# Performance work log

Hardware: AMD Instinct MI355X
Metric: run time of the kernel (lower is better)

Reference implementation:

```python
import jax, jax.numpy as jnp
import numpy as np

DELTA = 1e-6  # small constant used throughout the original repo


def _theta(memory, keys):
    # batchwise cosine similarity: memory [b,m,w], keys [b,r,w] -> [b,r,m]
    a = memory / (jnp.linalg.norm(memory, axis=2, keepdims=True) + DELTA)
    b = keys / (jnp.linalg.norm(keys, axis=2, keepdims=True) + DELTA)
    return jnp.einsum('bmw,brw->brm', a, b)


def _content_weightings(memory, keys, strengths):
    d = _theta(memory, keys)                       # [b,r,m]
    s = jax.nn.softplus(strengths)[..., None]      # [b,r,1]
    return jax.nn.softmax(d * s, axis=2)


def _allocate(usage):
    # usage [b,m]
    u = DELTA + (1.0 - DELTA) * usage
    phi = jnp.argsort(u, axis=1)                          # ascending, like topk(largest=False)
    sorted_u = jnp.take_along_axis(u, phi, axis=1)
    sorted_alloc = (1.0 - sorted_u) * jnp.cumprod(sorted_u, axis=1)  # fake_cumprod == inclusive cumprod
    alloc = jnp.take_along_axis(sorted_alloc, phi, axis=1)           # faithful to .gather(1, phi) in source
    return alloc[:, None, :]                              # [b,1,m]


def _dnc_step(xi, W, bW, memory, link_matrix, precedence, read_weights, write_weights, usage_vector):
    b, m, w = memory.shape
    r = read_weights.shape[1]
    iface = xi @ W + bW                                   # [b, r*w + 3*w + 5*r + 3]
    i0 = r * w
    read_keys = iface[:, :i0].reshape(b, r, w)
    read_strengths = 1.0 + jax.nn.relu(iface[:, i0:i0 + r])              # [b,r]
    write_key = iface[:, i0 + r:i0 + r + w].reshape(b, 1, w)
    write_strength = (1.0 + jax.nn.relu(iface[:, i0 + r + w]))[:, None]  # [b,1]
    erase_vector = jax.nn.sigmoid(iface[:, i0 + r + w + 1:i0 + r + 2 * w + 1]).reshape(b, 1, w)
    write_vector = iface[:, i0 + r + 2 * w + 1:i0 + r + 3 * w + 1].reshape(b, 1, w)
    free_gates = jax.nn.sigmoid(iface[:, i0 + r + 3 * w + 1:i0 + 2 * r + 3 * w + 1])  # [b,r]
    allocation_gate = jax.nn.sigmoid(iface[:, i0 + 2 * r + 3 * w + 1])[:, None]       # [b,1]
    write_gate = jax.nn.sigmoid(iface[:, i0 + 2 * r + 3 * w + 2])[:, None]            # [b,1]
    # NOTE: source slices read_modes starting at the write_gate index (faithful) and softmaxes over dim 1
    read_modes = jax.nn.softmax(iface[:, i0 + 2 * r + 3 * w + 2:i0 + 5 * r + 3 * w + 2].reshape(b, r, 3), axis=1)

    # ---- write path ----
    usage = usage_vector + (1.0 - usage_vector) * (1.0 - jnp.prod(1.0 - write_weights, axis=1))
    psi = jnp.prod(1.0 - free_gates[:, :, None] * read_weights, axis=1)  # [b,m]
    usage = usage * psi

    write_content_w = _content_weightings(memory, write_key, write_strength)  # [b,1,m]
    alloc = _allocate(usage)                                                  # [b,1,m]
    ag = allocation_gate[:, :, None]
    wg = write_gate[:, :, None]
    new_write_w = wg * (ag * alloc + (1.0 - ag) * write_content_w)            # [b,1,m]

    weighted_resets = new_write_w[:, :, :, None] * erase_vector[:, :, None, :]  # [b,1,m,w]
    reset_gate = jnp.prod(1.0 - weighted_resets, axis=1)                        # [b,m,w]
    new_memory = memory * reset_gate + jnp.einsum('bkm,bkw->bmw', new_write_w, write_vector)

    prec4 = precedence[:, :, None, :]            # [b,1,1,m]
    ww_i = new_write_w[:, :, :, None]            # [b,1,m,1]
    ww_j = new_write_w[:, :, None, :]            # [b,1,1,m]
    new_link = (1.0 - ww_i - ww_j) * link_matrix + ww_i * prec4
    new_link = new_link * (1.0 - jnp.eye(m, dtype=memory.dtype))[None, None]

    new_prec = (1.0 - jnp.sum(new_write_w, axis=2, keepdims=True)) * precedence + new_write_w

    # ---- read path ----
    content_w = _content_weightings(new_memory, read_keys, read_strengths)  # [b,r,m]
    forward_w = jnp.einsum('bkmn,brn->brkm', new_link, read_weights)        # [b,r,1,m]
    backward_w = jnp.einsum('brm,bkmn->brkn', read_weights, new_link)       # [b,r,1,m]
    content_mode = read_modes[:, :, 2:3] * content_w
    backward_mode = jnp.sum(read_modes[:, :, 0:1, None] * backward_w, axis=2)
    forward_mode = jnp.sum(read_modes[:, :, 1:2, None] * forward_w, axis=2)
    new_read_w = backward_mode + content_mode + forward_mode                # [b,r,m]

    read_vectors = jnp.einsum('brm,bmw->brw', new_read_w, new_memory)       # [b,r,w]
    return read_vectors


def setup_inputs() -> dict:
    key = jax.random.key(0)
    ks = jax.random.split(key, 3)
    b, m, w, r, d = 64, 1024, 64, 4, 512
    iface_size = r * w + 3 * w + 5 * r + 3  # 471
    return {
        'xi': jax.random.normal(ks[0], (b, d), dtype=jnp.float32),
        'W': jax.random.normal(ks[1], (d, iface_size), dtype=jnp.float32) * 0.05,
        'bW': jnp.zeros((iface_size,), dtype=jnp.float32),
        'memory': jnp.zeros((b, m, w), dtype=jnp.float32),
        'link_matrix': jnp.zeros((b, 1, m, m), dtype=jnp.float32),
        'precedence': jnp.zeros((b, 1, m), dtype=jnp.float32),
        'read_weights': jnp.zeros((b, r, m), dtype=jnp.float32),
        'write_weights': jnp.zeros((b, 1, m), dtype=jnp.float32),
        'usage_vector': jnp.zeros((b, m), dtype=jnp.float32),
    }


def reference(xi, W, bW, memory, link_matrix, precedence, read_weights, write_weights, usage_vector):
    return _dnc_step(xi, W, bW, memory, link_matrix, precedence, read_weights, write_weights, usage_vector)
```

## Files before the change

kernel.cpp:

```cpp
#include <hip/hip_runtime.h>

#define DELTA 1e-6f

#define NB 64
#define NM 1024
#define NW 64
#define NR 4
#define ND 512
#define NIF 471

typedef unsigned long long ull;

__device__ __forceinline__ float sigmoidf_(float x){ return 1.0f/(1.0f+expf(-x)); }
__device__ __forceinline__ float softplusf_(float x){ return fmaxf(x,0.0f) + log1pf(expf(-fabsf(x))); }

__device__ __forceinline__ float waveSum(float v){
  #pragma unroll
  for(int o=32;o>0;o>>=1) v += __shfl_down(v,o,64);
  return v;
}
__device__ __forceinline__ float waveMax(float v){
  #pragma unroll
  for(int o=32;o>0;o>>=1) v = fmaxf(v, __shfl_down(v,o,64));
  return v;
}
__device__ __forceinline__ ull shflxor64(ull k, int m){
  unsigned lo = (unsigned)(k & 0xffffffffu), hi = (unsigned)(k>>32);
  lo = (unsigned)__shfl_xor((int)lo, m, 64);
  hi = (unsigned)__shfl_xor((int)hi, m, 64);
  return ((ull)hi<<32)|lo;
}

__global__ __launch_bounds__(256) void k_zero(float4* __restrict__ p, int n4){
  int i = blockIdx.x*256 + threadIdx.x;
  if (i < n4) p[i] = make_float4(0.f,0.f,0.f,0.f);
}

__global__ __launch_bounds__(256) void k_iface(const float* __restrict__ xi,
                                               const float* __restrict__ Wm,
                                               const float* __restrict__ bW,
                                               float* __restrict__ iface){
  int b = blockIdx.x, half = blockIdx.y;
  __shared__ float xs[ND];
  for(int k=threadIdx.x;k<ND;k+=256) xs[k]=xi[b*ND+k];
  __syncthreads();
  int c = half*236 + threadIdx.x;
  int cend = half ? NIF : 236;
  if (c < cend){
    float acc = bW[c];
    #pragma unroll 4
    for(int k=0;k<ND;k++) acc = fmaf(xs[k], Wm[k*NIF+c], acc);
    iface[b*NIF+c]=acc;
  }
}

__global__ __launch_bounds__(256) void k_wcos(
    const float* __restrict__ iface, const float* __restrict__ mem,
    const float* __restrict__ rw_old, const float* __restrict__ ww_old,
    const float* __restrict__ uv,
    float* __restrict__ uu, float* __restrict__ wcd, float* __restrict__ wcn){
  int b = blockIdx.y;
  int j = blockIdx.x*256 + threadIdx.x;
  __shared__ float wkey[NW];
  const float* ifb = iface + b*NIF;
  if (threadIdx.x < NW) wkey[threadIdx.x] = ifb[260+threadIdx.x];
  __syncthreads();
  float fg0=sigmoidf_(ifb[453]), fg1=sigmoidf_(ifb[454]);
  float fg2=sigmoidf_(ifb[455]), fg3=sigmoidf_(ifb[456]);
  float u0  = uv[b*NM+j];
  float wwo = ww_old[b*NM+j];
  float usage = u0 + (1.0f-u0)*wwo;
  float psi = (1.0f - fg0*rw_old[(b*NR+0)*NM+j])
            * (1.0f - fg1*rw_old[(b*NR+1)*NM+j])
            * (1.0f - fg2*rw_old[(b*NR+2)*NM+j])
            * (1.0f - fg3*rw_old[(b*NR+3)*NM+j]);
  usage *= psi;
  uu[b*NM+j] = DELTA + (1.0f-DELTA)*usage;
  float dot=0.0f, nrm=0.0f;
  const float4* mrow4 = (const float4*)(mem + ((size_t)b*NM + j)*NW);
  #pragma unroll 4
  for(int k=0;k<16;k++){
    float4 mv = mrow4[k];
    const float* wk = wkey + k*4;
    dot = fmaf(mv.x,wk[0],dot); dot = fmaf(mv.y,wk[1],dot);
    dot = fmaf(mv.z,wk[2],dot); dot = fmaf(mv.w,wk[3],dot);
    nrm = fmaf(mv.x,mv.x,nrm); nrm = fmaf(mv.y,mv.y,nrm);
    nrm = fmaf(mv.z,mv.z,nrm); nrm = fmaf(mv.w,mv.w,nrm);
  }
  wcd[b*NM+j]=dot; wcn[b*NM+j]=nrm;
}

__global__ __launch_bounds__(1024) void k_write2(
    const float* __restrict__ iface, const float* __restrict__ uu,
    const float* __restrict__ wcd, const float* __restrict__ wcn,
    float* __restrict__ wwp){
  int b = blockIdx.x; int tid = threadIdx.x;
  int lane = tid & 63, wv = tid >> 6;
  __shared__ float wkey[NW];
  __shared__ ull skA[NM];
  __shared__ ull skB[NM];
  __shared__ float fb2[NM];
  __shared__ float red[17];
  __shared__ float s_wp[16], s_wp2[16];
  const float* ifb = iface + b*NIF;
  if (tid < NW) wkey[tid] = ifb[260+tid];
  __syncthreads();
  float sw = softplusf_(1.0f + fmaxf(ifb[324],0.0f));
  float ag = sigmoidf_(ifb[457]);
  float wg = sigmoidf_(ifb[458]);
  float kn=0.0f;
  for(int k=0;k<NW;k++){ float t=wkey[k]; kn += t*t; }
  kn = sqrtf(kn);
  float logit = sw * wcd[b*NM+tid] / ((sqrtf(wcn[b*NM+tid])+DELTA)*(kn+DELTA));
  float m1 = waveMax(logit); if(lane==0) red[wv]=m1; __syncthreads();
  if(tid==0){ float mm=red[0]; for(int i=1;i<16;i++) mm=fmaxf(mm,red[i]); red[16]=mm; } __syncthreads();
  float e = expf(logit - red[16]);
  float s1 = waveSum(e); if(lane==0) red[wv]=s1; __syncthreads();
  if(tid==0){ float ss=0; for(int i=0;i<16;i++) ss+=red[i]; red[16]=ss; } __syncthreads();
  float wcw = e/red[16];
  float u = uu[b*NM+tid];
  ull k = ((ull)__float_as_uint(u) << 32) | (unsigned)tid;
  bool useA = true;
  for (int k2=2; k2<=NM; k2<<=1){
    for (int jj=k2>>1; jj>0; jj>>=1){
      ull p;
      if (jj >= 64){
        ull* buf = useA ? skA : skB;
        buf[tid] = k;
        __syncthreads();
        p = buf[tid^jj];
        useA = !useA;
      } else {
        p = shflxor64(k, jj);
      }
      bool lower = (tid & jj) == 0;
      bool asc   = (tid & k2) == 0;
      bool takeMin = (lower == asc);
      k = takeMin ? (k<p ? k : p) : (k>p ? k : p);
    }
  }
  float su = __uint_as_float((unsigned)(k>>32));
  int phi  = (int)(k & 0xffffffffu);
  float sc = su;
  #pragma unroll
  for (int off=1; off<64; off<<=1){
    float t = __shfl_up(sc, off, 64);
    if (lane >= off) sc *= t;
  }
  if (lane==63) s_wp[wv] = sc;
  __syncthreads();
  if (tid==0){
    float p=1.0f;
    for (int w=0;w<16;w++){ float t=s_wp[w]; s_wp2[w]=p; p*=t; }
  }
  __syncthreads();
  float P = sc * s_wp2[wv];
  float salloc = (1.0f - su)*P;
  fb2[phi] = salloc;
  __syncthreads();
  float alloc = fb2[tid];
  wwp[b*NM+tid] = wg*(ag*alloc + (1.0f-ag)*wcw);
}

__global__ __launch_bounds__(256) void k_link8(
    const float* __restrict__ link, const float* __restrict__ rw,
    const float* __restrict__ wwp,
    float4* __restrict__ RFp, float* __restrict__ C2p, float* __restrict__ C3p,
    float* __restrict__ ldiag){
  int cx = blockIdx.x, ry = blockIdx.y, b = blockIdx.z;
  int tid = threadIdx.x, lane = tid&63, wv = tid>>6;
  __shared__ float4 s_L4[32*64];
  __shared__ float4 s_gcol4[256];
  __shared__ float  s_mwc[256];
  __shared__ float4 s_grow4[32];
  __shared__ float  s_wwr[32];
  __shared__ float4 s_rfp4[128];
  const float* Lb = link + ((size_t)b<<20);
  int colbase = cx*256, rowbase = ry*256;
  {
    float g0 = rw[(b*NR+0)*NM + colbase + tid];
    float g1 = rw[(b*NR+1)*NM + colbase + tid];
    float g2 = rw[(b*NR+2)*NM + colbase + tid];
    float g3 = rw[(b*NR+3)*NM + colbase + tid];
    s_gcol4[tid] = make_float4(g0,g1,g2,g3);
    s_mwc[tid] = 1.0f - wwp[b*NM + colbase + tid];
  }
  float c2a[NR][4], c3a[NR][4];
  #pragma unroll
  for(int r=0;r<NR;r++){
    #pragma unroll
    for(int e=0;e<4;e++){ c2a[r][e]=0.0f; c3a[r][e]=0.0f; }
  }
  for (int ch=0; ch<8; ++ch){
    int rb = rowbase + ch*32;
    if (tid < 128) ((float*)s_grow4)[tid] = rw[(b*NR+(tid&3))*NM + rb + (tid>>2)];
    if (tid < 32)  s_wwr[tid] = wwp[b*NM + rb + tid];
    #pragma unroll
    for (int jq=0;jq<8;jq++){
      int rl = wv + 4*jq;
      float4 lv = *(const float4*)(Lb + (size_t)(rb+rl)*NM + colbase + lane*4);
      s_L4[rl*64 + (lane ^ ((rl>>1)&7))] = lv;
    }
    __syncthreads();
    if (cx == ry && tid < 32){
      int coff = ch*32 + tid;
      float4 v = s_L4[tid*64 + ((coff>>2) ^ ((tid>>1)&7))];
      float d = (coff&1) ? ((coff&2)? v.w : v.y) : ((coff&2)? v.z : v.x);
      ldiag[b*NM + rb + tid] = d;
    }
    {
      int i5 = lane & 15, cg = lane >> 4;
      int rl0 = 2*i5;
      int sz = i5 & 7;
      float wwj0 = s_wwr[rl0], wwj1 = s_wwr[rl0+1];
      float rf0[4] = {0,0,0,0}, rf1[4] = {0,0,0,0};
      #pragma unroll
      for (int q=0;q<4;q++){
        int cq = wv*16 + cg*4 + q;
        float4 mw  = ((const float4*)s_mwc)[cq];
        float4 lv0 = s_L4[rl0*64 + (cq ^ sz)];
        float4 lv1 = s_L4[(rl0+1)*64 + (cq ^ sz)];
        float le0[4]={lv0.x,lv0.y,lv0.z,lv0.w};
        float le1[4]={lv1.x,lv1.y,lv1.z,lv1.w};
        float mv[4]={mw.x,mw.y,mw.z,mw.w};
        #pragma unroll
        for (int e=0;e<4;e++){
          float4 gv = s_gcol4[cq*4+e];
          float lt0 = le0[e]*(mv[e]-wwj0);
          float lt1 = le1[e]*(mv[e]-wwj1);
          rf0[0]=fmaf(lt0,gv.x,rf0[0]); rf0[1]=fmaf(lt0,gv.y,rf0[1]);
          rf0[2]=fmaf(lt0,gv.z,rf0[2]); rf0[3]=fmaf(lt0,gv.w,rf0[3]);
          rf1[0]=fmaf(lt1,gv.x,rf1[0]); rf1[1]=fmaf(lt1,gv.y,rf1[1]);
          rf1[2]=fmaf(lt1,gv.z,rf1[2]); rf1[3]=fmaf(lt1,gv.w,rf1[3]);
        }
      }
      #pragma unroll
      for (int r=0;r<NR;r++){
        rf0[r] += __shfl_xor(rf0[r], 16, 64);
        rf0[r] += __shfl_xor(rf0[r], 32, 64);
        rf1[r] += __shfl_xor(rf1[r], 16, 64);
        rf1[r] += __shfl_xor(rf1[r], 32, 64);
      }
      if (cg == 0){
        s_rfp4[wv*32 + rl0]     = make_float4(rf0[0],rf0[1],rf0[2],rf0[3]);
        s_rfp4[wv*32 + rl0 + 1] = make_float4(rf1[0],rf1[1],rf1[2],rf1[3]);
      }
    }
    #pragma unroll 2
    for (int ri=0; ri<8; ri++){
      int row = wv*8 + ri;
      float4 lv = s_L4[row*64 + (lane ^ ((row>>1)&7))];
      float4 gg = s_grow4[row];
      float wwr = s_wwr[row];
      float le[4] = {lv.x,lv.y,lv.z,lv.w};
      float ggv[4] = {gg.x,gg.y,gg.z,gg.w};
      float ggw[4];
      #pragma unroll
      for (int r=0;r<NR;r++) ggw[r] = ggv[r]*wwr;
      #pragma unroll
      for (int e=0;e<4;e++){
        #pragma unroll
        for (int r=0;r<NR;r++){
          c2a[r][e] = fmaf(le[e], ggv[r], c2a[r][e]);
          c3a[r][e] = fmaf(le[e], ggw[r], c3a[r][e]);
        }
      }
    }
    __syncthreads();
    if (tid < 128){
      int row = tid>>2, r = tid&3;
      float s = ((const float*)&s_rfp4[0*32+row])[r] + ((const float*)&s_rfp4[1*32+row])[r]
              + ((const float*)&s_rfp4[2*32+row])[r] + ((const float*)&s_rfp4[3*32+row])[r];
      ((float*)RFp)[((size_t)cx<<18) + (b*NM + rb + row)*4 + r] = s;
    }
    __syncthreads();
  }
  float4* s_comb = s_L4;
  #pragma unroll
  for (int r=0;r<NR;r++){
    s_comb[tid*8 + r]     = make_float4(c2a[r][0],c2a[r][1],c2a[r][2],c2a[r][3]);
    s_comb[tid*8 + 4 + r] = make_float4(c3a[r][0],c3a[r][1],c3a[r][2],c3a[r][3]);
  }
  __syncthreads();
  for (int t=tid; t<512; t+=256){
    int lc = t>>3, q = t&7;
    float4 a = s_comb[(0*64+lc)*8+q];
    float4 bb= s_comb[(1*64+lc)*8+q];
    float4 c = s_comb[(2*64+lc)*8+q];
    float4 d = s_comb[(3*64+lc)*8+q];
    float4 s = make_float4(a.x+bb.x+c.x+d.x, a.y+bb.y+c.y+d.y, a.z+bb.z+c.z+d.z, a.w+bb.w+c.w+d.w);
    float* dst = (q<4) ? &C2p[((size_t)ry<<18) + (b*NR+q)*NM + colbase + lc*4]
                       : &C3p[((size_t)ry<<18) + (b*NR+(q-4))*NM + colbase + lc*4];
    *(float4*)dst = s;
  }
}

__global__ __launch_bounds__(256) void k_rdots(
    const float* __restrict__ iface, const float* __restrict__ mem,
    const float* __restrict__ wwp, float* __restrict__ dots){
  int b = blockIdx.y;
  int j = blockIdx.x*256 + threadIdx.x;
  __shared__ float keys[NR][NW];
  __shared__ float er[NW], wvec[NW];
  const float* ifb = iface + b*NIF;
  { int r=threadIdx.x>>6, kk=threadIdx.x&63; keys[r][kk] = ifb[r*NW+kk]; }
  if (threadIdx.x < 64) er[threadIdx.x] = sigmoidf_(ifb[325+threadIdx.x]);
  else if (threadIdx.x < 128) wvec[threadIdx.x-64] = ifb[389+threadIdx.x-64];
  __syncthreads();
  float wwj = wwp[b*NM+j];
  const float* mrow = mem + ((size_t)b*NM+j)*NW;
  float dt[NR]={0,0,0,0}; float nrm=0.0f;
  for(int k=0;k<NW;k++){
    float nmv = fmaf(mrow[k], (1.0f - wwj*er[k]), wwj*wvec[k]);
    nrm = fmaf(nmv,nmv,nrm);
    #pragma unroll
    for(int r=0;r<NR;r++) dt[r] = fmaf(nmv, keys[r][k], dt[r]);
  }
  #pragma unroll
  for(int r=0;r<NR;r++) dots[(b*5+r)*NM + j] = dt[r];
  dots[(b*5+4)*NM + j] = nrm;
}

__global__ __launch_bounds__(1024) void k_rmid(
    const float* __restrict__ iface, const float* __restrict__ prec,
    const float* __restrict__ rw_old, const float* __restrict__ wwp,
    const float* __restrict__ dots, const float* __restrict__ ldiag,
    const float4* __restrict__ RFp4, const float* __restrict__ C2p, const float* __restrict__ C3p,
    float* __restrict__ nrwg){
  int b = blockIdx.x; int tid = threadIdx.x; int lane=tid&63, wv=tid>>6;
  __shared__ float s_pk[16][8];
  __shared__ float scal[16];
  __shared__ float smax[NR], ssum[NR];
  __shared__ float rm[NR][3];
  const float* ifb = iface + b*NIF;
  if (tid == 0){
    for(int mo=0;mo<3;mo++){
      float x0=ifb[458+0*3+mo], x1=ifb[458+1*3+mo], x2=ifb[458+2*3+mo], x3=ifb[458+3*3+mo];
      float mx = fmaxf(fmaxf(x0,x1),fmaxf(x2,x3));
      float e0=expf(x0-mx),e1=expf(x1-mx),e2=expf(x2-mx),e3=expf(x3-mx);
      float s=e0+e1+e2+e3;
      rm[0][mo]=e0/s; rm[1][mo]=e1/s; rm[2][mo]=e2/s; rm[3][mo]=e3/s;
    }
  }
  if (tid >= 320 && tid < 324){
    int r = tid-320;
    float knv=0;
    for(int k=0;k<NW;k++){ float t=ifb[r*NW+k]; knv += t*t; }
    scal[8+r]  = sqrtf(knv);
    scal[12+r] = softplusf_(1.0f + fmaxf(ifb[256+r],0.0f));
  }
  __syncthreads();
  int j = tid;
  float pj  = prec[b*NM+j];
  float wwj = wwp[b*NM+j];
  float rwv[NR];
  #pragma unroll
  for(int r=0;r<NR;r++) rwv[r]=rw_old[(b*NR+r)*NM+j];
  {
    float v8[8];
    #pragma unroll
    for(int r=0;r<NR;r++){ v8[r] = pj*rwv[r]; v8[4+r] = wwj*rwv[r]; }
    #pragma unroll
    for(int q=0;q<8;q++){
      float s = waveSum(v8[q]);
      if(lane==0) s_pk[wv][q]=s;
    }
    __syncthreads();
    if (tid < 8){
      float ss=0;
      for(int w=0;w<16;w++) ss += s_pk[w][tid];
      scal[tid]=ss;
    }
    __syncthreads();
  }
  float dt[NR];
  #pragma unroll
  for(int r=0;r<NR;r++) dt[r] = dots[(b*5+r)*NM + j];
  float nrm = dots[(b*5+4)*NM + j];
  float inv = 1.0f/(sqrtf(nrm)+DELTA);
  float logit[NR], ce[NR], cw[NR];
  #pragma unroll
  for(int r=0;r<NR;r++) logit[r] = scal[12+r]*dt[r]*inv/(scal[8+r]+DELTA);
  #pragma unroll
  for(int r=0;r<NR;r++){
    float m1 = waveMax(logit[r]);
    if(lane==0) s_pk[wv][r]=m1;
  }
  __syncthreads();
  if (tid < NR){
    float mm=s_pk[0][tid];
    for(int w=1;w<16;w++) mm=fmaxf(mm,s_pk[w][tid]);
    smax[tid]=mm;
  }
  __syncthreads();
  #pragma unroll
  for(int r=0;r<NR;r++){
    ce[r] = expf(logit[r]-smax[r]);
    float s1 = waveSum(ce[r]);
    if(lane==0) s_pk[wv][r]=s1;
  }
  __syncthreads();
  if (tid < NR){
    float ss=0;
    for(int w=0;w<16;w++) ss += s_pk[w][tid];
    ssum[tid]=ss;
  }
  __syncthreads();
  #pragma unroll
  for(int r=0;r<NR;r++) cw[r] = ce[r]/ssum[r];
  float Ljj = ldiag[b*NM+j];
  float4 Fa = RFp4[(0<<16) + b*NM + j];
  float4 Fb = RFp4[(1<<16) + b*NM + j];
  float4 Fc = RFp4[(2<<16) + b*NM + j];
  float4 Fd = RFp4[(3<<16) + b*NM + j];
  float Fr[4] = {Fa.x+Fb.x+Fc.x+Fd.x, Fa.y+Fb.y+Fc.y+Fd.y,
                 Fa.z+Fb.z+Fc.z+Fd.z, Fa.w+Fb.w+Fc.w+Fd.w};
  #pragma unroll
  for(int r=0;r<NR;r++){
    int idx = (b*NR+r)*NM + j;
    float cc2 = C2p[idx] + C2p[262144+idx] + C2p[524288+idx] + C2p[786432+idx];
    float cc3 = C3p[idx] + C3p[262144+idx] + C3p[524288+idx] + C3p[786432+idx];
    float F   = Fr[r];
    float grj = rwv[r];
    float fwd = F - Ljj*grj*(1.0f-2.0f*wwj) + wwj*(scal[r] - pj*grj);
    float bwd = (cc2 - cc3) - Ljj*grj*(1.0f-wwj) - wwj*(cc2 - Ljj*grj) + pj*(scal[4+r] - wwj*grj);
    nrwg[(b*NR+r)*NM+j] = rm[r][0]*bwd + rm[r][1]*fwd + rm[r][2]*cw[r];
  }
}

__global__ __launch_bounds__(256) void k_readb(
    const float* __restrict__ iface, const float* __restrict__ mem,
    const float* __restrict__ wwp, const float* __restrict__ nrwg,
    float* __restrict__ out){
  int jt = blockIdx.x, b = blockIdx.y;
  int tid = threadIdx.x, lane = tid&63, wv = tid>>6;
  __shared__ float s_nrw[NR][256];
  __shared__ float s_ww[256];
  __shared__ float s_er[NW], s_wv[NW];
  __shared__ float s_acc[4][NR][NW];
  const float* ifb = iface + b*NIF;
  int j0 = jt*256;
  #pragma unroll
  for(int r=0;r<NR;r++) s_nrw[r][tid] = nrwg[(b*NR+r)*NM + j0+tid];
  s_ww[tid] = wwp[b*NM + j0+tid];
  if (tid < 64) s_er[tid] = sigmoidf_(ifb[325+tid]);
  else if (tid < 128) s_wv[tid-64] = ifb[389+tid-64];
  __syncthreads();
  int w = lane;
  float erw = s_er[w], wvw = s_wv[w];
  float acc[NR]={0,0,0,0};
  for(int jj=0;jj<64;jj++){
    int jl = wv*64+jj;
    float wwr = s_ww[jl];
    float nmv = fmaf(mem[((size_t)b*NM + j0+jl)*NW + w], (1.0f - wwr*erw), wwr*wvw);
    #pragma unroll
    for(int r=0;r<NR;r++) acc[r] = fmaf(s_nrw[r][jl], nmv, acc[r]);
  }
  #pragma unroll
  for(int r=0;r<NR;r++) s_acc[wv][r][w] = acc[r];
  __syncthreads();
  {
    int r = tid>>6, k = tid&63;
    float s = s_acc[0][r][k]+s_acc[1][r][k]+s_acc[2][r][k]+s_acc[3][r][k];
    atomicAdd(&out[b*NR*NW + r*NW + k], s);
  }
}

extern "C" void kernel_launch(void* const* d_in, const int* in_sizes, int n_in,
                              void* d_out, int out_size, void* d_ws, size_t ws_size,
                              hipStream_t stream) {
  (void)in_sizes; (void)n_in; (void)out_size; (void)ws_size;
  const float* xi   = (const float*)d_in[0];
  const float* Wm   = (const float*)d_in[1];
  const float* bW   = (const float*)d_in[2];
  const float* mem  = (const float*)d_in[3];
  const float* link = (const float*)d_in[4];
  const float* prec = (const float*)d_in[5];
  const float* rw   = (const float*)d_in[6];
  const float* wwo  = (const float*)d_in[7];
  const float* uv   = (const float*)d_in[8];
  float* out = (float*)d_out;
  float* ws  = (float*)d_ws;
  float* iface = ws;
  float* wwp   = ws + 30208;
  float* uu    = ws + 95744;
  float* wcd   = ws + 161280;
  float* wcn   = ws + 226816;
  float* dots  = ws + 292352;
  float* ldiag = ws + 620032;
  float* nrwg  = ws + 685568;
  float* RFp   = ws + 947712;
  float* C2p   = ws + 1996288;
  float* C3p   = ws + 3044864;
  k_zero <<<16, 256, 0, stream>>>((float4*)out, 4096);
  k_iface<<<dim3(NB,2), 256, 0, stream>>>(xi, Wm, bW, iface);
  k_wcos <<<dim3(4,NB), 256, 0, stream>>>(iface, mem, rw, wwo, uv, uu, wcd, wcn);
  k_write2<<<NB, 1024, 0, stream>>>(iface, uu, wcd, wcn, wwp);
  k_link8<<<dim3(4,4,NB), 256, 0, stream>>>(link, rw, wwp, (float4*)RFp, C2p, C3p, ldiag);
  k_rdots<<<dim3(4,NB), 256, 0, stream>>>(iface, mem, wwp, dots);
  k_rmid <<<NB, 1024, 0, stream>>>(iface, prec, rw, wwp, dots, ldiag, (const float4*)RFp, C2p, C3p, nrwg);
  k_readb<<<dim3(4,NB), 256, 0, stream>>>(iface, mem, wwp, nrwg, out);
}
```

Before: 158.6 us.

## Fuse read-dot and output-zero kernels into link kernel with smaller row chunks

Merges the k_rdots and k_zero launches into the link kernel by adding an extra grid slice (blockIdx.y==4) that computes memory-key dot products and zeroes the output. The link tile loop now processes 16-row chunks instead of 32, preloads all row gates and write weights once, and halves shared-memory use for the link tile. This removes two launches, lets the dot-product blocks overlap with link work, and raises occupancy, at the cost of more loop iterations and barriers per block.

```diff
diff --git a/kernel.cpp b/kernel.cpp
--- a/kernel.cpp
+++ b/kernel.cpp
@@ -29,11 +29,6 @@
   lo = (unsigned)__shfl_xor((int)lo, m, 64);
   hi = (unsigned)__shfl_xor((int)hi, m, 64);
   return ((ull)hi<<32)|lo;
-}
-
-__global__ __launch_bounds__(256) void k_zero(float4* __restrict__ p, int n4){
-  int i = blockIdx.x*256 + threadIdx.x;
-  if (i < n4) p[i] = make_float4(0.f,0.f,0.f,0.f);
 }
 
 __global__ __launch_bounds__(256) void k_iface(const float* __restrict__ xi,
@@ -162,19 +157,49 @@
   wwp[b*NM+tid] = wg*(ag*alloc + (1.0f-ag)*wcw);
 }
 
-__global__ __launch_bounds__(256) void k_link8(
+__global__ __launch_bounds__(256) void k_linkr(
     const float* __restrict__ link, const float* __restrict__ rw,
     const float* __restrict__ wwp,
-    float4* __restrict__ RFp, float* __restrict__ C2p, float* __restrict__ C3p,
-    float* __restrict__ ldiag){
-  int cx = blockIdx.x, ry = blockIdx.y, b = blockIdx.z;
-  int tid = threadIdx.x, lane = tid&63, wv = tid>>6;
-  __shared__ float4 s_L4[32*64];
+    float* __restrict__ RFp, float* __restrict__ C2p, float* __restrict__ C3p,
+    float* __restrict__ ldiag,
+    const float* __restrict__ iface, const float* __restrict__ mem,
+    float* __restrict__ dots, float4* __restrict__ out4){
+  __shared__ float4 s_L4[16*64];
   __shared__ float4 s_gcol4[256];
   __shared__ float  s_mwc[256];
-  __shared__ float4 s_grow4[32];
-  __shared__ float  s_wwr[32];
-  __shared__ float4 s_rfp4[128];
+  __shared__ float4 s_grow4[256];
+  __shared__ float  s_wwr[256];
+  __shared__ float4 s_rfp4[4][16];
+  __shared__ float  s_keys[NR][NW];
+  __shared__ float  s_er[NW], s_wvec[NW];
+  int tid = threadIdx.x, lane = tid&63, wv = tid>>6;
+  int b = blockIdx.z;
+
+  if (blockIdx.y == 4){
+    int jt = blockIdx.x;
+    if (jt == 0 && b < 16) out4[b*256 + tid] = make_float4(0.f,0.f,0.f,0.f);
+    const float* ifb = iface + b*NIF;
+    { int r=tid>>6, kk=tid&63; s_keys[r][kk] = ifb[r*NW+kk]; }
+    if (tid < 64) s_er[tid] = sigmoidf_(ifb[325+tid]);
+    else if (tid < 128) s_wvec[tid-64] = ifb[389+tid-64];
+    __syncthreads();
+    int j = jt*256 + tid;
+    float wwj = wwp[b*NM+j];
+    const float* mrow = mem + ((size_t)b*NM+j)*NW;
+    float dt[NR]={0,0,0,0}; float nrm=0.0f;
+    for(int k=0;k<NW;k++){
+      float nmv = fmaf(mrow[k], (1.0f - wwj*s_er[k]), wwj*s_wvec[k]);
+      nrm = fmaf(nmv,nmv,nrm);
+      #pragma unroll
+      for(int r=0;r<NR;r++) dt[r] = fmaf(nmv, s_keys[r][k], dt[r]);
+    }
+    #pragma unroll
+    for(int r=0;r<NR;r++) dots[(b*5+r)*NM + j] = dt[r];
+    dots[(b*5+4)*NM + j] = nrm;
+    return;
+  }
+
+  int cx = blockIdx.x, ry = blockIdx.y;
   const float* Lb = link + ((size_t)b<<20);
   int colbase = cx*256, rowbase = ry*256;
   {
@@ -184,6 +209,9 @@
     float g3 = rw[(b*NR+3)*NM + colbase + tid];
     s_gcol4[tid] = make_float4(g0,g1,g2,g3);
     s_mwc[tid] = 1.0f - wwp[b*NM + colbase + tid];
+    for (int t=tid; t<1024; t+=256)
+      ((float*)s_grow4)[t] = rw[(b*NR+(t&3))*NM + rowbase + (t>>2)];
+    s_wwr[tid] = wwp[b*NM + rowbase + tid];
   }
   float c2a[NR][4], c3a[NR][4];
   #pragma unroll
@@ -191,67 +219,56 @@
     #pragma unroll
     for(int e=0;e<4;e++){ c2a[r][e]=0.0f; c3a[r][e]=0.0f; }
   }
-  for (int ch=0; ch<8; ++ch){
-    int rb = rowbase + ch*32;
-    if (tid < 128) ((float*)s_grow4)[tid] = rw[(b*NR+(tid&3))*NM + rb + (tid>>2)];
-    if (tid < 32)  s_wwr[tid] = wwp[b*NM + rb + tid];
-    #pragma unroll
-    for (int jq=0;jq<8;jq++){
+  const bool isdiag = (cx==ry);
+  for (int ch=0; ch<16; ++ch){
+    int rb = rowbase + ch*16;
+    #pragma unroll
+    for (int jq=0;jq<4;jq++){
       int rl = wv + 4*jq;
+      int sz = (rl>>1)&7;
       float4 lv = *(const float4*)(Lb + (size_t)(rb+rl)*NM + colbase + lane*4);
-      s_L4[rl*64 + (lane ^ ((rl>>1)&7))] = lv;
+      s_L4[rl*64 + (lane ^ sz)] = lv;
     }
     __syncthreads();
-    if (cx == ry && tid < 32){
-      int coff = ch*32 + tid;
-      float4 v = s_L4[tid*64 + ((coff>>2) ^ ((tid>>1)&7))];
+    if (isdiag && tid < 16){
+      int lr = tid, coff = ch*16 + lr, cq = coff>>2;
+      float4 v = s_L4[lr*64 + (cq ^ ((lr>>1)&7))];
       float d = (coff&1) ? ((coff&2)? v.w : v.y) : ((coff&2)? v.z : v.x);
-      ldiag[b*NM + rb + tid] = d;
+      ldiag[b*NM + rb + lr] = d;
     }
     {
       int i5 = lane & 15, cg = lane >> 4;
-      int rl0 = 2*i5;
-      int sz = i5 & 7;
-      float wwj0 = s_wwr[rl0], wwj1 = s_wwr[rl0+1];
-      float rf0[4] = {0,0,0,0}, rf1[4] = {0,0,0,0};
+      int sz = (i5>>1)&7;
+      float wwj = s_wwr[ch*16 + i5];
+      float rf[4] = {0,0,0,0};
       #pragma unroll
       for (int q=0;q<4;q++){
         int cq = wv*16 + cg*4 + q;
-        float4 mw  = ((const float4*)s_mwc)[cq];
-        float4 lv0 = s_L4[rl0*64 + (cq ^ sz)];
-        float4 lv1 = s_L4[(rl0+1)*64 + (cq ^ sz)];
-        float le0[4]={lv0.x,lv0.y,lv0.z,lv0.w};
-        float le1[4]={lv1.x,lv1.y,lv1.z,lv1.w};
+        float4 mw = ((const float4*)s_mwc)[cq];
+        float4 lv = s_L4[i5*64 + (cq ^ sz)];
+        float le[4]={lv.x,lv.y,lv.z,lv.w};
         float mv[4]={mw.x,mw.y,mw.z,mw.w};
         #pragma unroll
         for (int e=0;e<4;e++){
           float4 gv = s_gcol4[cq*4+e];
-          float lt0 = le0[e]*(mv[e]-wwj0);
-          float lt1 = le1[e]*(mv[e]-wwj1);
-          rf0[0]=fmaf(lt0,gv.x,rf0[0]); rf0[1]=fmaf(lt0,gv.y,rf0[1]);
-          rf0[2]=fmaf(lt0,gv.z,rf0[2]); rf0[3]=fmaf(lt0,gv.w,rf0[3]);
-          rf1[0]=fmaf(lt1,gv.x,rf1[0]); rf1[1]=fmaf(lt1,gv.y,rf1[1]);
-          rf1[2]=fmaf(lt1,gv.z,rf1[2]); rf1[3]=fmaf(lt1,gv.w,rf1[3]);
+          float lt = le[e]*(mv[e]-wwj);
+          rf[0]=fmaf(lt,gv.x,rf[0]); rf[1]=fmaf(lt,gv.y,rf[1]);
+          rf[2]=fmaf(lt,gv.z,rf[2]); rf[3]=fmaf(lt,gv.w,rf[3]);
         }
       }
       #pragma unroll
       for (int r=0;r<NR;r++){
-        rf0[r] += __shfl_xor(rf0[r], 16, 64);
-        rf0[r] += __shfl_xor(rf0[r], 32, 64);
-        rf1[r] += __shfl_xor(rf1[r], 16, 64);
-        rf1[r] += __shfl_xor(rf1[r], 32, 64);
+        rf[r] += __shfl_xor(rf[r], 16, 64);
+        rf[r] += __shfl_xor(rf[r], 32, 64);
       }
-      if (cg == 0){
-        s_rfp4[wv*32 + rl0]     = make_float4(rf0[0],rf0[1],rf0[2],rf0[3]);
-        s_rfp4[wv*32 + rl0 + 1] = make_float4(rf1[0],rf1[1],rf1[2],rf1[3]);
-      }
-    }
-    #pragma unroll 2
-    for (int ri=0; ri<8; ri++){
-      int row = wv*8 + ri;
+      if (cg == 0) s_rfp4[wv][i5] = make_float4(rf[0],rf[1],rf[2],rf[3]);
+    }
+    #pragma unroll
+    for (int ri=0; ri<4; ri++){
+      int row = wv*4 + ri;
       float4 lv = s_L4[row*64 + (lane ^ ((row>>1)&7))];
-      float4 gg = s_grow4[row];
-      float wwr = s_wwr[row];
+      float4 gg = s_grow4[ch*16+row];
+      float wwr = s_wwr[ch*16+row];
       float le[4] = {lv.x,lv.y,lv.z,lv.w};
       float ggv[4] = {gg.x,gg.y,gg.z,gg.w};
       float ggw[4];
@@ -267,58 +284,40 @@
       }
     }
     __syncthreads();
-    if (tid < 128){
+    if (tid < 64){
       int row = tid>>2, r = tid&3;
-      float s = ((const float*)&s_rfp4[0*32+row])[r] + ((const float*)&s_rfp4[1*32+row])[r]
-              + ((const float*)&s_rfp4[2*32+row])[r] + ((const float*)&s_rfp4[3*32+row])[r];
-      ((float*)RFp)[((size_t)cx<<18) + (b*NM + rb + row)*4 + r] = s;
-    }
-    __syncthreads();
-  }
+      float s = ((const float*)&s_rfp4[0][row])[r] + ((const float*)&s_rfp4[1][row])[r]
+              + ((const float*)&s_rfp4[2][row])[r] + ((const float*)&s_rfp4[3][row])[r];
+      RFp[((size_t)cx<<18) + (size_t)(b*NM + rb + row)*4 + r] = s;
+    }
+  }
+  __syncthreads();
   float4* s_comb = s_L4;
   #pragma unroll
-  for (int r=0;r<NR;r++){
-    s_comb[tid*8 + r]     = make_float4(c2a[r][0],c2a[r][1],c2a[r][2],c2a[r][3]);
-    s_comb[tid*8 + 4 + r] = make_float4(c3a[r][0],c3a[r][1],c3a[r][2],c3a[r][3]);
-  }
-  __syncthreads();
-  for (int t=tid; t<512; t+=256){
-    int lc = t>>3, q = t&7;
-    float4 a = s_comb[(0*64+lc)*8+q];
-    float4 bb= s_comb[(1*64+lc)*8+q];
-    float4 c = s_comb[(2*64+lc)*8+q];
-    float4 d = s_comb[(3*64+lc)*8+q];
+  for (int r=0;r<NR;r++) s_comb[tid*4 + r] = make_float4(c2a[r][0],c2a[r][1],c2a[r][2],c2a[r][3]);
+  __syncthreads();
+  {
+    int lc = tid>>2, r = tid&3;
+    float4 a = s_comb[(0*64+lc)*4+r];
+    float4 bb= s_comb[(1*64+lc)*4+r];
+    float4 c = s_comb[(2*64+lc)*4+r];
+    float4 d = s_comb[(3*64+lc)*4+r];
     float4 s = make_float4(a.x+bb.x+c.x+d.x, a.y+bb.y+c.y+d.y, a.z+bb.z+c.z+d.z, a.w+bb.w+c.w+d.w);
-    float* dst = (q<4) ? &C2p[((size_t)ry<<18) + (b*NR+q)*NM + colbase + lc*4]
-                       : &C3p[((size_t)ry<<18) + (b*NR+(q-4))*NM + colbase + lc*4];
-    *(float4*)dst = s;
-  }
-}
-
-__global__ __launch_bounds__(256) void k_rdots(
-    const float* __restrict__ iface, const float* __restrict__ mem,
-    const float* __restrict__ wwp, float* __restrict__ dots){
-  int b = blockIdx.y;
-  int j = blockIdx.x*256 + threadIdx.x;
-  __shared__ float keys[NR][NW];
-  __shared__ float er[NW], wvec[NW];
-  const float* ifb = iface + b*NIF;
-  { int r=threadIdx.x>>6, kk=threadIdx.x&63; keys[r][kk] = ifb[r*NW+kk]; }
-  if (threadIdx.x < 64) er[threadIdx.x] = sigmoidf_(ifb[325+threadIdx.x]);
-  else if (threadIdx.x < 128) wvec[threadIdx.x-64] = ifb[389+threadIdx.x-64];
-  __syncthreads();
-  float wwj = wwp[b*NM+j];
-  const float* mrow = mem + ((size_t)b*NM+j)*NW;
-  float dt[NR]={0,0,0,0}; float nrm=0.0f;
-  for(int k=0;k<NW;k++){
-    float nmv = fmaf(mrow[k], (1.0f - wwj*er[k]), wwj*wvec[k]);
-    nrm = fmaf(nmv,nmv,nrm);
-    #pragma unroll
-    for(int r=0;r<NR;r++) dt[r] = fmaf(nmv, keys[r][k], dt[r]);
-  }
-  #pragma unroll
-  for(int r=0;r<NR;r++) dots[(b*5+r)*NM + j] = dt[r];
-  dots[(b*5+4)*NM + j] = nrm;
+    *(float4*)&C2p[((size_t)blockIdx.y<<18) + (b*NR+r)*NM + colbase + lc*4] = s;
+  }
+  __syncthreads();
+  #pragma unroll
+  for (int r=0;r<NR;r++) s_comb[tid*4 + r] = make_float4(c3a[r][0],c3a[r][1],c3a[r][2],c3a[r][3]);
+  __syncthreads();
+  {
+    int lc = tid>>2, r = tid&3;
+    float4 a = s_comb[(0*64+lc)*4+r];
+    float4 bb= s_comb[(1*64+lc)*4+r];
+    float4 c = s_comb[(2*64+lc)*4+r];
+    float4 d = s_comb[(3*64+lc)*4+r];
+    float4 s = make_float4(a.x+bb.x+c.x+d.x, a.y+bb.y+c.y+d.y, a.z+bb.z+c.z+d.z, a.w+bb.w+c.w+d.w);
+    *(float4*)&C3p[((size_t)blockIdx.y<<18) + (b*NR+r)*NM + colbase + lc*4] = s;
+  }
 }
 
 __global__ __launch_bounds__(1024) void k_rmid(
@@ -492,12 +491,11 @@
   float* RFp   = ws + 947712;
   float* C2p   = ws + 1996288;
   float* C3p   = ws + 3044864;
-  k_zero <<<16, 256, 0, stream>>>((float4*)out, 4096);
   k_iface<<<dim3(NB,2), 256, 0, stream>>>(xi, Wm, bW, iface);
   k_wcos <<<dim3(4,NB), 256, 0, stream>>>(iface, mem, rw, wwo, uv, uu, wcd, wcn);
   k_write2<<<NB, 1024, 0, stream>>>(iface, uu, wcd, wcn, wwp);
-  k_link8<<<dim3(4,4,NB), 256, 0, stream>>>(link, rw, wwp, (float4*)RFp, C2p, C3p, ldiag);
-  k_rdots<<<dim3(4,NB), 256, 0, stream>>>(iface, mem, wwp, dots);
+  k_linkr<<<dim3(4,5,NB), 256, 0, stream>>>(link, rw, wwp, RFp, C2p, C3p, ldiag,
+                                            iface, mem, dots, (float4*)out);
   k_rmid <<<NB, 1024, 0, stream>>>(iface, prec, rw, wwp, dots, ldiag, (const float4*)RFp, C2p, C3p, nrwg);
   k_readb<<<dim3(4,NB), 256, 0, stream>>>(iface, mem, wwp, nrwg, out);
 }
```

Result: no change. 161.7 us (+1.9%).

## Fuse read-weight mid stage into read kernel and drop zero kernel

Applied to the files above, without the earlier changes.

Removes the separate zeroing kernel by clearing the output inside the interface matmul kernel. The per-batch 1024-thread k_rmid kernel is eliminated: the dots kernel now computes unnormalised content exponentials and accumulates the per-batch sums atomically. The read kernel then forms the new read weights directly in shared memory before the memory read. The content softmax drops max-subtraction, which risks overflow for large logits but saves a reduction pass. This cuts two launches and an intermediate buffer round-trip.

```diff
diff --git a/kernel.cpp b/kernel.cpp
--- a/kernel.cpp
+++ b/kernel.cpp
@@ -31,17 +31,14 @@
   return ((ull)hi<<32)|lo;
 }
 
-__global__ __launch_bounds__(256) void k_zero(float4* __restrict__ p, int n4){
-  int i = blockIdx.x*256 + threadIdx.x;
-  if (i < n4) p[i] = make_float4(0.f,0.f,0.f,0.f);
-}
-
 __global__ __launch_bounds__(256) void k_iface(const float* __restrict__ xi,
                                                const float* __restrict__ Wm,
                                                const float* __restrict__ bW,
-                                               float* __restrict__ iface){
+                                               float* __restrict__ iface,
+                                               float4* __restrict__ out4){
   int b = blockIdx.x, half = blockIdx.y;
   __shared__ float xs[ND];
+  if (half == 0 && threadIdx.x < 64) out4[b*64 + threadIdx.x] = make_float4(0.f,0.f,0.f,0.f);
   for(int k=threadIdx.x;k<ND;k+=256) xs[k]=xi[b*ND+k];
   __syncthreads();
   int c = half*236 + threadIdx.x;
@@ -93,7 +90,7 @@
 __global__ __launch_bounds__(1024) void k_write2(
     const float* __restrict__ iface, const float* __restrict__ uu,
     const float* __restrict__ wcd, const float* __restrict__ wcn,
-    float* __restrict__ wwp){
+    float* __restrict__ wwp, float* __restrict__ sPK){
   int b = blockIdx.x; int tid = threadIdx.x;
   int lane = tid & 63, wv = tid >> 6;
   __shared__ float wkey[NW];
@@ -104,6 +101,7 @@
   __shared__ float s_wp[16], s_wp2[16];
   const float* ifb = iface + b*NIF;
   if (tid < NW) wkey[tid] = ifb[260+tid];
+  if (tid < 16) sPK[b*16+tid] = 0.0f;
   __syncthreads();
   float sw = softplusf_(1.0f + fmaxf(ifb[324],0.0f));
   float ag = sigmoidf_(ifb[457]);
@@ -295,19 +293,31 @@
   }
 }
 
-__global__ __launch_bounds__(256) void k_rdots(
+__global__ __launch_bounds__(256) void k_rdots2(
     const float* __restrict__ iface, const float* __restrict__ mem,
-    const float* __restrict__ wwp, float* __restrict__ dots){
-  int b = blockIdx.y;
-  int j = blockIdx.x*256 + threadIdx.x;
+    const float* __restrict__ wwp, const float* __restrict__ prec,
+    const float* __restrict__ rw_old,
+    float* __restrict__ ce, float* __restrict__ sPK){
+  int b = blockIdx.y, jt = blockIdx.x;
+  int tid = threadIdx.x, lane = tid&63, wv = tid>>6;
   __shared__ float keys[NR][NW];
   __shared__ float er[NW], wvec[NW];
+  __shared__ float sk[NR];
+  __shared__ float red[4][12];
   const float* ifb = iface + b*NIF;
-  { int r=threadIdx.x>>6, kk=threadIdx.x&63; keys[r][kk] = ifb[r*NW+kk]; }
-  if (threadIdx.x < 64) er[threadIdx.x] = sigmoidf_(ifb[325+threadIdx.x]);
-  else if (threadIdx.x < 128) wvec[threadIdx.x-64] = ifb[389+threadIdx.x-64];
-  __syncthreads();
+  { int r=tid>>6, kk=tid&63; keys[r][kk] = ifb[r*NW+kk]; }
+  if (tid < 64) er[tid] = sigmoidf_(ifb[325+tid]);
+  else if (tid < 128) wvec[tid-64] = ifb[389+tid-64];
+  else if (tid < 132){
+    int r = tid-128;
+    float knv=0;
+    for(int k=0;k<NW;k++){ float t=ifb[r*NW+k]; knv += t*t; }
+    sk[r] = softplusf_(1.0f + fmaxf(ifb[256+r],0.0f)) / (sqrtf(knv)+DELTA);
+  }
+  __syncthreads();
+  int j = jt*256 + tid;
   float wwj = wwp[b*NM+j];
+  float pj  = prec[b*NM+j];
   const float* mrow = mem + ((size_t)b*NM+j)*NW;
   float dt[NR]={0,0,0,0}; float nrm=0.0f;
   for(int k=0;k<NW;k++){
@@ -316,22 +326,44 @@
     #pragma unroll
     for(int r=0;r<NR;r++) dt[r] = fmaf(nmv, keys[r][k], dt[r]);
   }
-  #pragma unroll
-  for(int r=0;r<NR;r++) dots[(b*5+r)*NM + j] = dt[r];
-  dots[(b*5+4)*NM + j] = nrm;
-}
-
-__global__ __launch_bounds__(1024) void k_rmid(
-    const float* __restrict__ iface, const float* __restrict__ prec,
-    const float* __restrict__ rw_old, const float* __restrict__ wwp,
-    const float* __restrict__ dots, const float* __restrict__ ldiag,
+  float inv = 1.0f/(sqrtf(nrm)+DELTA);
+  float v12[12];
+  #pragma unroll
+  for(int r=0;r<NR;r++){
+    float e = expf(sk[r]*dt[r]*inv);
+    ce[(b*NR+r)*NM + j] = e;
+    float rwv = rw_old[(b*NR+r)*NM+j];
+    v12[r]   = pj*rwv;
+    v12[4+r] = wwj*rwv;
+    v12[8+r] = e;
+  }
+  #pragma unroll
+  for(int q=0;q<12;q++){
+    float s = waveSum(v12[q]);
+    if (lane==0) red[wv][q] = s;
+  }
+  __syncthreads();
+  if (tid < 12){
+    float s = red[0][tid]+red[1][tid]+red[2][tid]+red[3][tid];
+    atomicAdd(&sPK[b*16+tid], s);
+  }
+}
+
+__global__ __launch_bounds__(256) void k_readf(
+    const float* __restrict__ iface, const float* __restrict__ mem,
+    const float* __restrict__ wwp, const float* __restrict__ prec,
+    const float* __restrict__ rw_old, const float* __restrict__ ldiag,
     const float4* __restrict__ RFp4, const float* __restrict__ C2p, const float* __restrict__ C3p,
-    float* __restrict__ nrwg){
-  int b = blockIdx.x; int tid = threadIdx.x; int lane=tid&63, wv=tid>>6;
-  __shared__ float s_pk[16][8];
-  __shared__ float scal[16];
-  __shared__ float smax[NR], ssum[NR];
+    const float* __restrict__ ce, const float* __restrict__ sPK,
+    float* __restrict__ out){
+  int jt = blockIdx.x, b = blockIdx.y;
+  int tid = threadIdx.x, lane = tid&63, wv = tid>>6;
+  __shared__ float s_nrw[NR][256];
+  __shared__ float s_ww[256];
+  __shared__ float s_er[NW], s_wv[NW];
+  __shared__ float s_acc[4][NR][NW];
   __shared__ float rm[NR][3];
+  __shared__ float s_sc[16];
   const float* ifb = iface + b*NIF;
   if (tid == 0){
     for(int mo=0;mo<3;mo++){
@@ -342,72 +374,15 @@
       rm[0][mo]=e0/s; rm[1][mo]=e1/s; rm[2][mo]=e2/s; rm[3][mo]=e3/s;
     }
   }
-  if (tid >= 320 && tid < 324){
-    int r = tid-320;
-    float knv=0;
-    for(int k=0;k<NW;k++){ float t=ifb[r*NW+k]; knv += t*t; }
-    scal[8+r]  = sqrtf(knv);
-    scal[12+r] = softplusf_(1.0f + fmaxf(ifb[256+r],0.0f));
-  }
-  __syncthreads();
-  int j = tid;
+  if (tid >= 64 && tid < 80)  s_sc[tid-64] = sPK[b*16 + (tid-64)];
+  if (tid >= 128 && tid < 192) s_er[tid-128] = sigmoidf_(ifb[325+tid-128]);
+  if (tid >= 192)              s_wv[tid-192] = ifb[389+tid-192];
+  int j0 = jt*256;
+  int j = j0 + tid;
+  float wwj = wwp[b*NM+j];
+  s_ww[tid] = wwj;
+  __syncthreads();
   float pj  = prec[b*NM+j];
-  float wwj = wwp[b*NM+j];
-  float rwv[NR];
-  #pragma unroll
-  for(int r=0;r<NR;r++) rwv[r]=rw_old[(b*NR+r)*NM+j];
-  {
-    float v8[8];
-    #pragma unroll
-    for(int r=0;r<NR;r++){ v8[r] = pj*rwv[r]; v8[4+r] = wwj*rwv[r]; }
-    #pragma unroll
-    for(int q=0;q<8;q++){
-      float s = waveSum(v8[q]);
-      if(lane==0) s_pk[wv][q]=s;
-    }
-    __syncthreads();
-    if (tid < 8){
-      float ss=0;
-      for(int w=0;w<16;w++) ss += s_pk[w][tid];
-      scal[tid]=ss;
-    }
-    __syncthreads();
-  }
-  float dt[NR];
-  #pragma unroll
-  for(int r=0;r<NR;r++) dt[r] = dots[(b*5+r)*NM + j];
-  float nrm = dots[(b*5+4)*NM + j];
-  float inv = 1.0f/(sqrtf(nrm)+DELTA);
-  float logit[NR], ce[NR], cw[NR];
-  #pragma unroll
-  for(int r=0;r<NR;r++) logit[r] = scal[12+r]*dt[r]*inv/(scal[8+r]+DELTA);
-  #pragma unroll
-  for(int r=0;r<NR;r++){
-    float m1 = waveMax(logit[r]);
-    if(lane==0) s_pk[wv][r]=m1;
-  }
-  __syncthreads();
-  if (tid < NR){
-    float mm=s_pk[0][tid];
-    for(int w=1;w<16;w++) mm=fmaxf(mm,s_pk[w][tid]);
-    smax[tid]=mm;
-  }
-  __syncthreads();
-  #pragma unroll
-  for(int r=0;r<NR;r++){
-    ce[r] = expf(logit[r]-smax[r]);
-    float s1 = waveSum(ce[r]);
-    if(lane==0) s_pk[wv][r]=s1;
-  }
-  __syncthreads();
-  if (tid < NR){
-    float ss=0;
-    for(int w=0;w<16;w++) ss += s_pk[w][tid];
-    ssum[tid]=ss;
-  }
-  __syncthreads();
-  #pragma unroll
-  for(int r=0;r<NR;r++) cw[r] = ce[r]/ssum[r];
   float Ljj = ldiag[b*NM+j];
   float4 Fa = RFp4[(0<<16) + b*NM + j];
   float4 Fb = RFp4[(1<<16) + b*NM + j];
@@ -420,31 +395,12 @@
     int idx = (b*NR+r)*NM + j;
     float cc2 = C2p[idx] + C2p[262144+idx] + C2p[524288+idx] + C2p[786432+idx];
     float cc3 = C3p[idx] + C3p[262144+idx] + C3p[524288+idx] + C3p[786432+idx];
-    float F   = Fr[r];
-    float grj = rwv[r];
-    float fwd = F - Ljj*grj*(1.0f-2.0f*wwj) + wwj*(scal[r] - pj*grj);
-    float bwd = (cc2 - cc3) - Ljj*grj*(1.0f-wwj) - wwj*(cc2 - Ljj*grj) + pj*(scal[4+r] - wwj*grj);
-    nrwg[(b*NR+r)*NM+j] = rm[r][0]*bwd + rm[r][1]*fwd + rm[r][2]*cw[r];
-  }
-}
-
-__global__ __launch_bounds__(256) void k_readb(
-    const float* __restrict__ iface, const float* __restrict__ mem,
-    const float* __restrict__ wwp, const float* __restrict__ nrwg,
-    float* __restrict__ out){
-  int jt = blockIdx.x, b = blockIdx.y;
-  int tid = threadIdx.x, lane = tid&63, wv = tid>>6;
-  __shared__ float s_nrw[NR][256];
-  __shared__ float s_ww[256];
-  __shared__ float s_er[NW], s_wv[NW];
-  __shared__ float s_acc[4][NR][NW];
-  const float* ifb = iface + b*NIF;
-  int j0 = jt*256;
-  #pragma unroll
-  for(int r=0;r<NR;r++) s_nrw[r][tid] = nrwg[(b*NR+r)*NM + j0+tid];
-  s_ww[tid] = wwp[b*NM + j0+tid];
-  if (tid < 64) s_er[tid] = sigmoidf_(ifb[325+tid]);
-  else if (tid < 128) s_wv[tid-64] = ifb[389+tid-64];
+    float grj = rw_old[idx];
+    float cwv = ce[idx] / s_sc[8+r];
+    float fwd = Fr[r] - Ljj*grj*(1.0f-2.0f*wwj) + wwj*(s_sc[r] - pj*grj);
+    float bwd = (cc2 - cc3) - Ljj*grj*(1.0f-wwj) - wwj*(cc2 - Ljj*grj) + pj*(s_sc[4+r] - wwj*grj);
+    s_nrw[r][tid] = rm[r][0]*bwd + rm[r][1]*fwd + rm[r][2]*cwv;
+  }
   __syncthreads();
   int w = lane;
   float erw = s_er[w], wvw = s_wv[w];
@@ -486,18 +442,17 @@
   float* uu    = ws + 95744;
   float* wcd   = ws + 161280;
   float* wcn   = ws + 226816;
-  float* dots  = ws + 292352;
-  float* ldiag = ws + 620032;
-  float* nrwg  = ws + 685568;
-  float* RFp   = ws + 947712;
-  float* C2p   = ws + 1996288;
-  float* C3p   = ws + 3044864;
-  k_zero <<<16, 256, 0, stream>>>((float4*)out, 4096);
-  k_iface<<<dim3(NB,2), 256, 0, stream>>>(xi, Wm, bW, iface);
+  float* ce    = ws + 292352;
+  float* ldiag = ws + 554496;
+  float* sPK   = ws + 620032;
+  float* RFp   = ws + 621056;
+  float* C2p   = ws + 1669632;
+  float* C3p   = ws + 2718208;
+  k_iface<<<dim3(NB,2), 256, 0, stream>>>(xi, Wm, bW, iface, (float4*)out);
   k_wcos <<<dim3(4,NB), 256, 0, stream>>>(iface, mem, rw, wwo, uv, uu, wcd, wcn);
-  k_write2<<<NB, 1024, 0, stream>>>(iface, uu, wcd, wcn, wwp);
+  k_write2<<<NB, 1024, 0, stream>>>(iface, uu, wcd, wcn, wwp, sPK);
   k_link8<<<dim3(4,4,NB), 256, 0, stream>>>(link, rw, wwp, (float4*)RFp, C2p, C3p, ldiag);
-  k_rdots<<<dim3(4,NB), 256, 0, stream>>>(iface, mem, wwp, dots);
-  k_rmid <<<NB, 1024, 0, stream>>>(iface, prec, rw, wwp, dots, ldiag, (const float4*)RFp, C2p, C3p, nrwg);
-  k_readb<<<dim3(4,NB), 256, 0, stream>>>(iface, mem, wwp, nrwg, out);
-}
+  k_rdots2<<<dim3(4,NB), 256, 0, stream>>>(iface, mem, wwp, prec, rw, ce, sPK);
+  k_readf<<<dim3(4,NB), 256, 0, stream>>>(iface, mem, wwp, prec, rw, ldiag,
+                                          (const float4*)RFp, C2p, C3p, ce, sPK, out);
+}
```

New measurement: 149.0 us, median of 2. 1.06x faster.
